# Optimization experiments

Hardware: AMD Instinct MI355X
Metric: run time of the kernel (lower is better)

Reference implementation:

```python
import jax, jax.numpy as jnp
import numpy as np

B, T, D, U = 32, 2048, 512, 512


def setup_inputs() -> dict:
    key = jax.random.key(0)
    ks = jax.random.split(key, 6)
    scale = 0.05
    return {
        "values": jax.random.normal(ks[0], (B, T, D), dtype=jnp.float32),
        "query": jax.random.normal(ks[1], (B, D), dtype=jnp.float32),
        "W1_w": jax.random.normal(ks[2], (D, U), dtype=jnp.float32) * scale,
        "W1_b": jnp.zeros((U,), dtype=jnp.float32),
        "W2_w": jax.random.normal(ks[3], (D, U), dtype=jnp.float32) * scale,
        "W2_b": jnp.zeros((U,), dtype=jnp.float32),
        "V_w": jax.random.normal(ks[4], (U, 1), dtype=jnp.float32) * scale,
        "V_b": jnp.zeros((1,), dtype=jnp.float32),
    }


def reference(values, query, W1_w, W1_b, W2_w, W2_b, V_w, V_b):
    # values: [B, T, D]; query: [B, D]
    proj_v = jnp.einsum("btd,du->btu", values, W1_w) + W1_b          # [B, T, U]
    proj_q = (query @ W2_w + W2_b)[:, None, :]                        # [B, 1, U]
    score = jnp.tanh(proj_v + proj_q) @ V_w + V_b                     # [B, T, 1]
    attention_weights = jax.nn.softmax(score, axis=1)                 # [B, T, 1]
    context_vector = jnp.sum(attention_weights * values, axis=1)      # [B, D]
    return context_vector, attention_weights
```

## Files before the change

kernel.cpp:

```cpp
#include <hip/hip_runtime.h>
#include <hip/hip_bf16.h>
#include <stdint.h>


#define B_DIM 32
#define T_DIM 2048
#define D_DIM 512
#define U_DIM 512
#define M_DIM (B_DIM * T_DIM)

typedef short bf16x8 __attribute__((ext_vector_type(8)));
typedef float f32x4 __attribute__((ext_vector_type(4)));

__device__ __forceinline__ short bf16r(float x) {
    unsigned u = __float_as_uint(x);
    u += 0x7fffu + ((u >> 16) & 1u);
    return (short)(u >> 16);
}

__device__ __forceinline__ bf16x8 pack_bf16x8(float4 a, float4 b) {
    bf16x8 r;
    r[0] = bf16r(a.x); r[1] = bf16r(a.y); r[2] = bf16r(a.z); r[3] = bf16r(a.w);
    r[4] = bf16r(b.x); r[5] = bf16r(b.y); r[6] = bf16r(b.z); r[7] = bf16r(b.w);
    return r;
}

__device__ __forceinline__ float fast_tanh(float x) {
    float e = __expf(2.0f * x);
    return 1.0f - __fdividef(2.0f, e + 1.0f);
}

__device__ __forceinline__ void g2lds16(const void* g, void* lds) {
    auto gp = reinterpret_cast<const __attribute__((address_space(1))) unsigned int*>(
        reinterpret_cast<uintptr_t>(g));
    auto lp = reinterpret_cast<__attribute__((address_space(3))) unsigned int*>(
        (unsigned int)(uintptr_t)lds);
    __builtin_amdgcn_global_load_lds(gp, lp, 16, 0, 0);
}


__global__ void prep_kernel(const float* __restrict__ W1_w,
                            const float* __restrict__ W1_b,
                            const float* __restrict__ W2_w,
                            const float* __restrict__ W2_b,
                            const float* __restrict__ query,
                            unsigned short* __restrict__ W1T,
                            float* __restrict__ qb) {
    __shared__ float red[256];
    const int tid = threadIdx.x;
    if (blockIdx.x < 128) {
        int n = blockIdx.x * 256 + tid;
        int u = n & 511;
        int c = n >> 9;
        bf16x8 pk;
#pragma unroll
        for (int j = 0; j < 8; ++j)
            pk[j] = bf16r(W1_w[(c * 8 + j) * U_DIM + u]);
        ((bf16x8*)W1T)[(u >> 5) * 2048 + c * 32 + (u & 31)] = pk;
    } else {
        int bid = blockIdx.x - 128;
        int b  = bid >> 3;
        int ug = bid & 7;
        int u  = ug * 64 + (tid & 63);
        int dq = tid >> 6;
        const float* q  = query + b * D_DIM + dq * 128;
        const float* w2 = W2_w + (size_t)(dq * 128) * U_DIM + u;
        float acc = 0.f;
#pragma unroll 8
        for (int d = 0; d < 128; ++d)
            acc += q[d] * w2[(size_t)d * U_DIM];
        red[tid] = acc;
        __syncthreads();
        if (tid < 64) {
            float s = red[tid] + red[tid + 64] + red[tid + 128] + red[tid + 192]
                    + W2_b[u] + W1_b[u];
            qb[b * U_DIM + u] = s;
        }
    }
}

__global__ __launch_bounds__(256, 2) void score_kernel(
        const float* __restrict__ values,
        const unsigned short* __restrict__ W1T,
        const float* __restrict__ qb,
        const float* __restrict__ Vw,
        float* __restrict__ scores) {
    __shared__ __align__(16) unsigned char smem[32 * 1024];

    const int tid  = threadIdx.x;
    const int lane = tid & 63;
    const int w    = tid >> 6;
    const int l15  = lane & 15;
    const int quad = lane >> 4;
    const int m0   = blockIdx.x * 128;
    const int b    = m0 >> 11;

#pragma unroll
    for (int i = 0; i < 8; ++i) {
        int unit = i * 256 + w * 64 + lane;
        g2lds16(W1T + (size_t)unit * 8, smem + (i * 256 + w * 64) * 16);
    }

    const int r0 = m0 + w * 32 + l15;
    const float* vrow0 = values + (size_t)r0 * D_DIM + quad * 8;
    const float* vrow1 = vrow0 + 16 * D_DIM;
    bf16x8 a0[16], a1[16];
#pragma unroll
    for (int ks = 0; ks < 16; ++ks) {
        float4 f0 = *(const float4*)(vrow0 + ks * 32);
        float4 f1 = *(const float4*)(vrow0 + ks * 32 + 4);
        a0[ks] = pack_bf16x8(f0, f1);
        float4 g0 = *(const float4*)(vrow1 + ks * 32);
        float4 g1 = *(const float4*)(vrow1 + ks * 32 + 4);
        a1[ks] = pack_bf16x8(g0, g1);
    }

    float sacc0[4] = {0.f, 0.f, 0.f, 0.f};
    float sacc1[4] = {0.f, 0.f, 0.f, 0.f};

    for (int uc = 0; uc < 16; ++uc) {
        __syncthreads();

        f32x4 acc0l = {0,0,0,0}, acc0h = {0,0,0,0};
        f32x4 acc1l = {0,0,0,0}, acc1h = {0,0,0,0};
        const unsigned char* bbase = smem + quad * 512 + l15 * 16;
#pragma unroll
        for (int ks = 0; ks < 16; ++ks) {
            bf16x8 blo = *(const bf16x8*)(bbase + ks * 2048);
            bf16x8 bhi = *(const bf16x8*)(bbase + ks * 2048 + 256);
            acc0l = __builtin_amdgcn_mfma_f32_16x16x32_bf16(a0[ks], blo, acc0l, 0, 0, 0);
            acc0h = __builtin_amdgcn_mfma_f32_16x16x32_bf16(a0[ks], bhi, acc0h, 0, 0, 0);
            acc1l = __builtin_amdgcn_mfma_f32_16x16x32_bf16(a1[ks], blo, acc1l, 0, 0, 0);
            acc1h = __builtin_amdgcn_mfma_f32_16x16x32_bf16(a1[ks], bhi, acc1h, 0, 0, 0);
        }

        const int u0 = uc * 32 + l15;
        const float qv0 = qb[b * U_DIM + u0];
        const float vw0 = Vw[u0];
        const float qv1 = qb[b * U_DIM + u0 + 16];
        const float vw1 = Vw[u0 + 16];
#pragma unroll
        for (int r = 0; r < 4; ++r) {
            sacc0[r] += fast_tanh(acc0l[r] + qv0) * vw0 + fast_tanh(acc0h[r] + qv1) * vw1;
            sacc1[r] += fast_tanh(acc1l[r] + qv0) * vw0 + fast_tanh(acc1h[r] + qv1) * vw1;
        }

        if (uc < 15) {
            __syncthreads();
            const unsigned short* src = W1T + (size_t)(uc + 1) * 32 * D_DIM;
#pragma unroll
            for (int i = 0; i < 8; ++i) {
                int unit = i * 256 + w * 64 + lane;
                g2lds16(src + (size_t)unit * 8, smem + (i * 256 + w * 64) * 16);
            }
        }
    }

#pragma unroll
    for (int r = 0; r < 4; ++r) {
        float v0 = sacc0[r], v1 = sacc1[r];
        v0 += __shfl_xor(v0, 1, 64); v1 += __shfl_xor(v1, 1, 64);
        v0 += __shfl_xor(v0, 2, 64); v1 += __shfl_xor(v1, 2, 64);
        v0 += __shfl_xor(v0, 4, 64); v1 += __shfl_xor(v1, 4, 64);
        v0 += __shfl_xor(v0, 8, 64); v1 += __shfl_xor(v1, 8, 64);
        sacc0[r] = v0; sacc1[r] = v1;
    }
    if (l15 == 0) {
        const int rowbase = m0 + w * 32 + quad * 4;
#pragma unroll
        for (int r = 0; r < 4; ++r) {
            scores[rowbase + r]      = sacc0[r];
            scores[rowbase + 16 + r] = sacc1[r];
        }
    }
}

__global__ void softmax_kernel(const float* __restrict__ scores,
                               float* __restrict__ out) {
    const int b = blockIdx.x;
    const int tid = threadIdx.x;

    out[b * D_DIM + tid] = 0.0f;
    out[b * D_DIM + 256 + tid] = 0.0f;

    float v[8];
    float mx = -1e30f;
#pragma unroll
    for (int i = 0; i < 8; ++i) {
        v[i] = scores[b * T_DIM + i * 256 + tid];
        mx = fmaxf(mx, v[i]);
    }
#pragma unroll
    for (int off = 1; off < 64; off <<= 1)
        mx = fmaxf(mx, __shfl_xor(mx, off, 64));
    __shared__ float redm[4];
    if ((tid & 63) == 0) redm[tid >> 6] = mx;
    __syncthreads();
    mx = fmaxf(fmaxf(redm[0], redm[1]), fmaxf(redm[2], redm[3]));

    float sum = 0.f;
#pragma unroll
    for (int i = 0; i < 8; ++i) {
        v[i] = __expf(v[i] - mx);
        sum += v[i];
    }
#pragma unroll
    for (int off = 1; off < 64; off <<= 1)
        sum += __shfl_xor(sum, off, 64);
    __shared__ float reds[4];
    if ((tid & 63) == 0) reds[tid >> 6] = sum;
    __syncthreads();
    sum = reds[0] + reds[1] + reds[2] + reds[3];

    const float inv = 1.0f / sum;
#pragma unroll
    for (int i = 0; i < 8; ++i)
        out[B_DIM * D_DIM + b * T_DIM + i * 256 + tid] = v[i] * inv;
}

__global__ void context_kernel(const float* __restrict__ values,
                               const float* __restrict__ weights,
                               float* __restrict__ ctx) {
    __shared__ float sw[128];
    const int tc = blockIdx.x;
    const int b  = blockIdx.y;
    const int tid = threadIdx.x;

    sw[tid] = weights[b * T_DIM + tc * 128 + tid];
    __syncthreads();

    const float4* vbase = (const float4*)(values + ((size_t)b * T_DIM + tc * 128) * D_DIM) + tid;
    float4 acc = {0.f, 0.f, 0.f, 0.f};
#pragma unroll 8
    for (int i = 0; i < 128; ++i) {
        float wv = sw[i];
        float4 v = vbase[(size_t)i * 128];
        acc.x += wv * v.x; acc.y += wv * v.y;
        acc.z += wv * v.z; acc.w += wv * v.w;
    }
    float* dst = ctx + b * D_DIM + tid * 4;
    atomicAdd(dst + 0, acc.x);
    atomicAdd(dst + 1, acc.y);
    atomicAdd(dst + 2, acc.z);
    atomicAdd(dst + 3, acc.w);
}

extern "C" void kernel_launch(void* const* d_in, const int* in_sizes, int n_in,
                              void* d_out, int out_size, void* d_ws, size_t ws_size,
                              hipStream_t stream) {
    const float* values = (const float*)d_in[0];
    const float* query  = (const float*)d_in[1];
    const float* W1_w   = (const float*)d_in[2];
    const float* W1_b   = (const float*)d_in[3];
    const float* W2_w   = (const float*)d_in[4];
    const float* W2_b   = (const float*)d_in[5];
    const float* V_w    = (const float*)d_in[6];

    float* out = (float*)d_out;

    unsigned char* ws = (unsigned char*)d_ws;
    unsigned short* W1T = (unsigned short*)(ws);
    float* qb     = (float*)(ws + 524288);
    float* scores = (float*)(ws + 524288 + 65536);

    prep_kernel<<<384, 256, 0, stream>>>(W1_w, W1_b, W2_w, W2_b, query, W1T, qb);
    score_kernel<<<M_DIM / 128, 256, 0, stream>>>(values, W1T, qb, V_w, scores);
    softmax_kernel<<<B_DIM, 256, 0, stream>>>(scores, out);
    context_kernel<<<dim3(16, B_DIM), 128, 0, stream>>>(values, out + B_DIM * D_DIM, out);
}
```

Measured before the change: 287.1 us.

## Retile score GEMM to 64x256 output tiles with K-streamed weights and partial-score slices

The score kernel now gives each block a 64-row by 256-unit tile and streams the K dimension through LDS one slice at a time, keeping accumulators for all units in registers. Partial scores from four column slices go to a workspace, and the softmax kernel sums them. The context kernel writes per-chunk partial sums that a new reduce kernel adds up, replacing the float atomics. Because the M-tile is split over two blocks, the values rows are now read twice. The change aims at better occupancy and less register pressure, at the cost of more launches and extra global traffic.

```diff
diff --git a/kernel.cpp b/kernel.cpp
--- a/kernel.cpp
+++ b/kernel.cpp
@@ -12,22 +12,24 @@
 typedef short bf16x8 __attribute__((ext_vector_type(8)));
 typedef float f32x4 __attribute__((ext_vector_type(4)));
 
+__device__ __forceinline__ float fast_tanh(float x) {
+    float e = __expf(2.0f * x);
+    return 1.0f - __fdividef(2.0f, e + 1.0f);
+}
+
 __device__ __forceinline__ short bf16r(float x) {
     unsigned u = __float_as_uint(x);
     u += 0x7fffu + ((u >> 16) & 1u);
     return (short)(u >> 16);
 }
 
-__device__ __forceinline__ bf16x8 pack_bf16x8(float4 a, float4 b) {
-    bf16x8 r;
-    r[0] = bf16r(a.x); r[1] = bf16r(a.y); r[2] = bf16r(a.z); r[3] = bf16r(a.w);
-    r[4] = bf16r(b.x); r[5] = bf16r(b.y); r[6] = bf16r(b.z); r[7] = bf16r(b.w);
-    return r;
-}
-
-__device__ __forceinline__ float fast_tanh(float x) {
-    float e = __expf(2.0f * x);
-    return 1.0f - __fdividef(2.0f, e + 1.0f);
+__device__ __forceinline__ bf16x8 pack8(float4 a, float4 b) {
+    union { __hip_bfloat162 h[4]; bf16x8 v; } u;
+    u.h[0] = __float22bfloat162_rn(make_float2(a.x, a.y));
+    u.h[1] = __float22bfloat162_rn(make_float2(a.z, a.w));
+    u.h[2] = __float22bfloat162_rn(make_float2(b.x, b.y));
+    u.h[3] = __float22bfloat162_rn(make_float2(b.z, b.w));
+    return u.v;
 }
 
 __device__ __forceinline__ void g2lds16(const void* g, void* lds) {
@@ -50,13 +52,17 @@
     const int tid = threadIdx.x;
     if (blockIdx.x < 128) {
         int n = blockIdx.x * 256 + tid;
-        int u = n & 511;
-        int c = n >> 9;
+        int uu    = n & 255;
+        int kc    = (n >> 8) & 3;
+        int kstep = (n >> 10) & 15;
+        int ut    = n >> 14;
+        int u  = ut * 256 + uu;
+        int k0 = kstep * 32 + kc * 8;
         bf16x8 pk;
 #pragma unroll
         for (int j = 0; j < 8; ++j)
-            pk[j] = bf16r(W1_w[(c * 8 + j) * U_DIM + u]);
-        ((bf16x8*)W1T)[(u >> 5) * 2048 + c * 32 + (u & 31)] = pk;
+            pk[j] = bf16r(W1_w[(size_t)(k0 + j) * U_DIM + u]);
+        ((bf16x8*)W1T)[n] = pk;
     } else {
         int bid = blockIdx.x - 128;
         int b  = bid >> 3;
@@ -72,9 +78,8 @@
         red[tid] = acc;
         __syncthreads();
         if (tid < 64) {
-            float s = red[tid] + red[tid + 64] + red[tid + 128] + red[tid + 192]
-                    + W2_b[u] + W1_b[u];
-            qb[b * U_DIM + u] = s;
+            qb[b * U_DIM + u] = red[tid] + red[tid + 64] + red[tid + 128]
+                              + red[tid + 192] + W2_b[u] + W1_b[u];
         }
     }
 }
@@ -84,110 +89,96 @@
         const unsigned short* __restrict__ W1T,
         const float* __restrict__ qb,
         const float* __restrict__ Vw,
-        float* __restrict__ scores) {
-    __shared__ __align__(16) unsigned char smem[32 * 1024];
+        float* __restrict__ sP) {
+    __shared__ __align__(16) unsigned char smem[16384];
 
     const int tid  = threadIdx.x;
     const int lane = tid & 63;
     const int w    = tid >> 6;
     const int l15  = lane & 15;
     const int quad = lane >> 4;
-    const int m0   = blockIdx.x * 128;
-    const int b    = m0 >> 11;
-
-#pragma unroll
-    for (int i = 0; i < 8; ++i) {
-        int unit = i * 256 + w * 64 + lane;
-        g2lds16(W1T + (size_t)unit * 8, smem + (i * 256 + w * 64) * 16);
-    }
-
-    const int r0 = m0 + w * 32 + l15;
-    const float* vrow0 = values + (size_t)r0 * D_DIM + quad * 8;
-    const float* vrow1 = vrow0 + 16 * D_DIM;
-    bf16x8 a0[16], a1[16];
-#pragma unroll
+    const int wr   = w >> 1, wc = w & 1;
+    const int ut    = blockIdx.x & 1;
+    const int mtile = blockIdx.x >> 1;
+    const int mb    = mtile * 64;
+    const int b     = mb >> 11;
+
+    const float* arow0 = values + (size_t)(mb + wr * 32 + l15) * D_DIM + quad * 8;
+    const float* arow1 = arow0 + 16 * D_DIM;
+
+    f32x4 acc[2][8] = {};
+
     for (int ks = 0; ks < 16; ++ks) {
-        float4 f0 = *(const float4*)(vrow0 + ks * 32);
-        float4 f1 = *(const float4*)(vrow0 + ks * 32 + 4);
-        a0[ks] = pack_bf16x8(f0, f1);
-        float4 g0 = *(const float4*)(vrow1 + ks * 32);
-        float4 g1 = *(const float4*)(vrow1 + ks * 32 + 4);
-        a1[ks] = pack_bf16x8(g0, g1);
-    }
-
-    float sacc0[4] = {0.f, 0.f, 0.f, 0.f};
-    float sacc1[4] = {0.f, 0.f, 0.f, 0.f};
-
-    for (int uc = 0; uc < 16; ++uc) {
+        float4 a00 = *(const float4*)(arow0 + ks * 32);
+        float4 a01 = *(const float4*)(arow0 + ks * 32 + 4);
+        float4 a10 = *(const float4*)(arow1 + ks * 32);
+        float4 a11 = *(const float4*)(arow1 + ks * 32 + 4);
+
         __syncthreads();
-
-        f32x4 acc0l = {0,0,0,0}, acc0h = {0,0,0,0};
-        f32x4 acc1l = {0,0,0,0}, acc1h = {0,0,0,0};
-        const unsigned char* bbase = smem + quad * 512 + l15 * 16;
-#pragma unroll
-        for (int ks = 0; ks < 16; ++ks) {
-            bf16x8 blo = *(const bf16x8*)(bbase + ks * 2048);
-            bf16x8 bhi = *(const bf16x8*)(bbase + ks * 2048 + 256);
-            acc0l = __builtin_amdgcn_mfma_f32_16x16x32_bf16(a0[ks], blo, acc0l, 0, 0, 0);
-            acc0h = __builtin_amdgcn_mfma_f32_16x16x32_bf16(a0[ks], bhi, acc0h, 0, 0, 0);
-            acc1l = __builtin_amdgcn_mfma_f32_16x16x32_bf16(a1[ks], blo, acc1l, 0, 0, 0);
-            acc1h = __builtin_amdgcn_mfma_f32_16x16x32_bf16(a1[ks], bhi, acc1h, 0, 0, 0);
-        }
-
-        const int u0 = uc * 32 + l15;
-        const float qv0 = qb[b * U_DIM + u0];
-        const float vw0 = Vw[u0];
-        const float qv1 = qb[b * U_DIM + u0 + 16];
-        const float vw1 = Vw[u0 + 16];
+        const unsigned short* src = W1T + (size_t)(ut * 16 + ks) * 8192;
+#pragma unroll
+        for (int i = 0; i < 4; ++i) {
+            int unit = i * 256 + w * 64 + lane;
+            g2lds16(src + (size_t)unit * 8, smem + unit * 16);
+        }
+        __syncthreads();
+
+        bf16x8 a0 = pack8(a00, a01);
+        bf16x8 a1 = pack8(a10, a11);
+        const unsigned char* bbase = smem + (size_t)(quad * 256 + wc * 128 + l15) * 16;
+#pragma unroll
+        for (int ui = 0; ui < 8; ++ui) {
+            bf16x8 bf = *(const bf16x8*)(bbase + ui * 256);
+            acc[0][ui] = __builtin_amdgcn_mfma_f32_16x16x32_bf16(a0, bf, acc[0][ui], 0, 0, 0);
+            acc[1][ui] = __builtin_amdgcn_mfma_f32_16x16x32_bf16(a1, bf, acc[1][ui], 0, 0, 0);
+        }
+    }
+
+    const int ub = ut * 256 + wc * 128 + l15;
+    float sm[2][4] = {};
+#pragma unroll
+    for (int ui = 0; ui < 8; ++ui) {
+        const int u = ub + ui * 16;
+        const float qv = qb[b * U_DIM + u];
+        const float vw = Vw[u];
+#pragma unroll
+        for (int mt = 0; mt < 2; ++mt)
+#pragma unroll
+            for (int r = 0; r < 4; ++r)
+                sm[mt][r] += fast_tanh(acc[mt][ui][r] + qv) * vw;
+    }
+#pragma unroll
+    for (int mt = 0; mt < 2; ++mt)
 #pragma unroll
         for (int r = 0; r < 4; ++r) {
-            sacc0[r] += fast_tanh(acc0l[r] + qv0) * vw0 + fast_tanh(acc0h[r] + qv1) * vw1;
-            sacc1[r] += fast_tanh(acc1l[r] + qv0) * vw0 + fast_tanh(acc1h[r] + qv1) * vw1;
-        }
-
-        if (uc < 15) {
-            __syncthreads();
-            const unsigned short* src = W1T + (size_t)(uc + 1) * 32 * D_DIM;
-#pragma unroll
-            for (int i = 0; i < 8; ++i) {
-                int unit = i * 256 + w * 64 + lane;
-                g2lds16(src + (size_t)unit * 8, smem + (i * 256 + w * 64) * 16);
-            }
-        }
-    }
-
-#pragma unroll
-    for (int r = 0; r < 4; ++r) {
-        float v0 = sacc0[r], v1 = sacc1[r];
-        v0 += __shfl_xor(v0, 1, 64); v1 += __shfl_xor(v1, 1, 64);
-        v0 += __shfl_xor(v0, 2, 64); v1 += __shfl_xor(v1, 2, 64);
-        v0 += __shfl_xor(v0, 4, 64); v1 += __shfl_xor(v1, 4, 64);
-        v0 += __shfl_xor(v0, 8, 64); v1 += __shfl_xor(v1, 8, 64);
-        sacc0[r] = v0; sacc1[r] = v1;
-    }
+            float v = sm[mt][r];
+            v += __shfl_xor(v, 1, 64);
+            v += __shfl_xor(v, 2, 64);
+            v += __shfl_xor(v, 4, 64);
+            v += __shfl_xor(v, 8, 64);
+            sm[mt][r] = v;
+        }
     if (l15 == 0) {
-        const int rowbase = m0 + w * 32 + quad * 4;
-#pragma unroll
-        for (int r = 0; r < 4; ++r) {
-            scores[rowbase + r]      = sacc0[r];
-            scores[rowbase + 16 + r] = sacc1[r];
-        }
-    }
-}
-
-__global__ void softmax_kernel(const float* __restrict__ scores,
+        const int slice = ut * 2 + wc;
+#pragma unroll
+        for (int mt = 0; mt < 2; ++mt)
+#pragma unroll
+            for (int r = 0; r < 4; ++r)
+                sP[slice * M_DIM + mb + wr * 32 + mt * 16 + quad * 4 + r] = sm[mt][r];
+    }
+}
+
+__global__ void softmax_kernel(const float* __restrict__ sP,
                                float* __restrict__ out) {
     const int b = blockIdx.x;
     const int tid = threadIdx.x;
 
-    out[b * D_DIM + tid] = 0.0f;
-    out[b * D_DIM + 256 + tid] = 0.0f;
-
     float v[8];
     float mx = -1e30f;
 #pragma unroll
     for (int i = 0; i < 8; ++i) {
-        v[i] = scores[b * T_DIM + i * 256 + tid];
+        int m = b * T_DIM + i * 256 + tid;
+        v[i] = sP[m] + sP[M_DIM + m] + sP[2 * M_DIM + m] + sP[3 * M_DIM + m];
         mx = fmaxf(mx, v[i]);
     }
 #pragma unroll
@@ -220,29 +211,45 @@
 
 __global__ void context_kernel(const float* __restrict__ values,
                                const float* __restrict__ weights,
-                               float* __restrict__ ctx) {
-    __shared__ float sw[128];
+                               float* __restrict__ P) {
+    __shared__ float sw[64];
+    __shared__ float red[512];
     const int tc = blockIdx.x;
     const int b  = blockIdx.y;
     const int tid = threadIdx.x;
-
-    sw[tid] = weights[b * T_DIM + tc * 128 + tid];
-    __syncthreads();
-
-    const float4* vbase = (const float4*)(values + ((size_t)b * T_DIM + tc * 128) * D_DIM) + tid;
+    const int d4 = tid & 127;
+    const int th = tid >> 7;
+
+    if (tid < 64) sw[tid] = weights[b * T_DIM + tc * 64 + tid];
+    __syncthreads();
+
+    const float4* vb = (const float4*)(values + ((size_t)b * T_DIM + tc * 64) * D_DIM) + d4;
     float4 acc = {0.f, 0.f, 0.f, 0.f};
 #pragma unroll 8
-    for (int i = 0; i < 128; ++i) {
+    for (int i = th; i < 64; i += 2) {
         float wv = sw[i];
-        float4 v = vbase[(size_t)i * 128];
-        acc.x += wv * v.x; acc.y += wv * v.y;
-        acc.z += wv * v.z; acc.w += wv * v.w;
-    }
-    float* dst = ctx + b * D_DIM + tid * 4;
-    atomicAdd(dst + 0, acc.x);
-    atomicAdd(dst + 1, acc.y);
-    atomicAdd(dst + 2, acc.z);
-    atomicAdd(dst + 3, acc.w);
+        float4 vv = vb[(size_t)i * 128];
+        acc.x += wv * vv.x; acc.y += wv * vv.y;
+        acc.z += wv * vv.z; acc.w += wv * vv.w;
+    }
+    if (th == 1) ((float4*)red)[d4] = acc;
+    __syncthreads();
+    if (th == 0) {
+        float4 o = ((float4*)red)[d4];
+        acc.x += o.x; acc.y += o.y; acc.z += o.z; acc.w += o.w;
+        *(float4*)(P + ((size_t)(b * 32 + tc)) * 512 + d4 * 4) = acc;
+    }
+}
+
+__global__ void reduce_kernel(const float* __restrict__ P,
+                              float* __restrict__ ctx) {
+    const int g = blockIdx.x * 256 + threadIdx.x;
+    const int b = g >> 9, d = g & 511;
+    float s = 0.f;
+#pragma unroll
+    for (int tc = 0; tc < 32; ++tc)
+        s += P[((size_t)(b * 32 + tc)) * 512 + d];
+    ctx[g] = s;
 }
 
 extern "C" void kernel_launch(void* const* d_in, const int* in_sizes, int n_in,
@@ -260,11 +267,13 @@
 
     unsigned char* ws = (unsigned char*)d_ws;
     unsigned short* W1T = (unsigned short*)(ws);
-    float* qb     = (float*)(ws + 524288);
-    float* scores = (float*)(ws + 524288 + 65536);
+    float* qb = (float*)(ws + 524288);
+    float* sP = (float*)(ws + 524288 + 65536);
+    float* P  = (float*)(ws + 524288 + 65536 + 1048576);
 
     prep_kernel<<<384, 256, 0, stream>>>(W1_w, W1_b, W2_w, W2_b, query, W1T, qb);
-    score_kernel<<<M_DIM / 128, 256, 0, stream>>>(values, W1T, qb, V_w, scores);
-    softmax_kernel<<<B_DIM, 256, 0, stream>>>(scores, out);
-    context_kernel<<<dim3(16, B_DIM), 128, 0, stream>>>(values, out + B_DIM * D_DIM, out);
-}
+    score_kernel<<<2048, 256, 0, stream>>>(values, W1T, qb, V_w, sP);
+    softmax_kernel<<<B_DIM, 256, 0, stream>>>(sP, out);
+    context_kernel<<<dim3(32, B_DIM), 256, 0, stream>>>(values, out + B_DIM * D_DIM, P);
+    reduce_kernel<<<64, 256, 0, stream>>>(P, out);
+}
```

Measured after the change: 292.8 us. No clear change (+2.0%).
